# Kernel optimization log

Measured on AMD Instinct MI355X. Metric: run time of the kernel, lower is better.

## Reference

```python
import jax, jax.numpy as jnp
import numpy as np

N_EXPERTS = 8
TOP_K = 2


def setup_inputs() -> dict:
    key = jax.random.key(0)
    ks = jax.random.split(key, 5)
    B, T, C, E, H = 8, 2048, 256, 8, 682  # H = int(8/3*256)
    scale = 1.0 / np.sqrt(C)
    return {
        "x": jax.random.normal(ks[0], (B, T, C), dtype=jnp.float32),
        "router_w": jax.random.normal(ks[1], (E, C), dtype=jnp.float32) * scale,
        "w1": jax.random.normal(ks[2], (E, H, C), dtype=jnp.float32) * scale,
        "w2": jax.random.normal(ks[3], (E, C, H), dtype=jnp.float32) * (1.0 / np.sqrt(H)),
        "w3": jax.random.normal(ks[4], (E, H, C), dtype=jnp.float32) * scale,
    }


def reference(x, router_w, w1, w2, w3):
    B, T, C = x.shape
    flat = x.reshape(-1, C)  # [N, C]

    # Router: softmax over experts, top-k selection, renormalize.
    logits = flat @ router_w.T                     # [N, E]
    probs = jax.nn.softmax(logits, axis=-1)
    topk_probs, topk_idx = jax.lax.top_k(probs, TOP_K)
    topk_probs = topk_probs / (jnp.sum(topk_probs, axis=-1, keepdims=True) + 1e-9)

    # Dense gate matrix [N, E]: zero for non-selected experts (same math as
    # the masked loop, since unselected experts contribute weight 0).
    onehot = jax.nn.one_hot(topk_idx, N_EXPERTS, dtype=flat.dtype)  # [N, K, E]
    gates = jnp.einsum("nk,nke->ne", topk_probs, onehot)           # [N, E]

    # SwiGLU experts, computed densely over E and combined with gates.
    h1 = jnp.einsum("nc,ehc->neh", flat, w1)       # [N, E, H]
    h3 = jnp.einsum("nc,ehc->neh", flat, w3)       # [N, E, H]
    h = jax.nn.silu(h1) * h3                       # [N, E, H]
    y = jnp.einsum("neh,ech->nec", h, w2)          # [N, E, C]
    out = jnp.einsum("ne,nec->nc", gates, y)       # [N, C]
    return out.reshape(B, T, C)
```

## Files before the change

kernel.cpp:

```cpp
#include <hip/hip_runtime.h>
#include <hip/hip_bf16.h>

#define N_TOK 16384
#define C_DIM 256
#define E_NUM 8
#define H_DIM 682
#define H_PAD 768
#define NROWS (N_TOK * 2)
#define HB 64
#define APB (NROWS / HB)

typedef short short8 __attribute__((ext_vector_type(8)));
typedef float floatx4 __attribute__((ext_vector_type(4)));
typedef unsigned int uint;

__device__ inline unsigned short f2bf(float v) {
    union { float f; uint u; } x; x.f = v;
    uint r = (x.u + 0x7fffu + ((x.u >> 16) & 1u)) >> 16;
    return (unsigned short)r;
}
__device__ inline float bf2f(unsigned short v) {
    union { uint u; float f; } x; x.u = ((uint)v) << 16; return x.f;
}

__device__ __forceinline__ void load_lds16(const void* g, void* l) {
    __builtin_amdgcn_global_load_lds(
        (const __attribute__((address_space(1))) unsigned int*)g,
        (__attribute__((address_space(3))) unsigned int*)l, 16, 0, 0);
}

#define VMCNT6 asm volatile("s_waitcnt vmcnt(6)" ::: "memory")
#define VMCNT4 asm volatile("s_waitcnt vmcnt(4)" ::: "memory")
#define VMCNT0 asm volatile("s_waitcnt vmcnt(0)" ::: "memory")

#define P13 (E_NUM * H_PAD * (C_DIM / 2))
#define P2  (E_NUM * C_DIM * (H_PAD / 2))
__global__ void wconvert(const float* __restrict__ w1, const float* __restrict__ w3,
                         const float* __restrict__ w2, unsigned short* __restrict__ w1b,
                         unsigned short* __restrict__ w3b, unsigned short* __restrict__ w2b) {
    int idx = blockIdx.x * 256 + threadIdx.x;
    if (idx < 2 * P13) {
        const float* src = (idx < P13) ? w1 : w3;
        unsigned short* dst = (idx < P13) ? w1b : w3b;
        int i = (idx < P13) ? idx : idx - P13;
        int e = i / (H_PAD * (C_DIM / 2));
        int rem = i - e * (H_PAD * (C_DIM / 2));
        int r = rem / (C_DIM / 2);
        int c2 = rem - r * (C_DIM / 2);
        uint v = 0;
        if (r < H_DIM) {
            const float2 f = *(const float2*)(src + ((size_t)e * H_DIM + r) * C_DIM + c2 * 2);
            v = (uint)f2bf(f.x) | ((uint)f2bf(f.y) << 16);
        }
        ((uint*)dst)[i] = v;
    } else if (idx < 2 * P13 + P2) {
        int i = idx - 2 * P13;
        int e = i / (C_DIM * (H_PAD / 2));
        int rem = i - e * (C_DIM * (H_PAD / 2));
        int r = rem / (H_PAD / 2);
        int c2 = rem - r * (H_PAD / 2);
        uint v = 0;
        if (c2 * 2 < H_DIM) {
            const float2 f = *(const float2*)(w2 + ((size_t)e * C_DIM + r) * H_DIM + c2 * 2);
            v = (uint)f2bf(f.x) | ((uint)f2bf(f.y) << 16);
        }
        ((uint*)w2b)[i] = v;
    }
}

__global__ __launch_bounds__(256) void router_kernel(
    const float* __restrict__ x, const float* __restrict__ rw,
    unsigned short* __restrict__ xb, int* __restrict__ as_e, float* __restrict__ as_gate) {
    __shared__ float rws[E_NUM * C_DIM];
    int tid = threadIdx.x;
    for (int i = tid; i < E_NUM * C_DIM; i += 256) rws[i] = rw[i];
    __syncthreads();
    int wave = tid >> 6, lane = tid & 63;
    int t = blockIdx.x * 4 + wave;
    const float4 xv = *(const float4*)(x + (size_t)t * C_DIM + lane * 4);
    uint2 pk;
    pk.x = (uint)f2bf(xv.x) | ((uint)f2bf(xv.y) << 16);
    pk.y = (uint)f2bf(xv.z) | ((uint)f2bf(xv.w) << 16);
    *(uint2*)(xb + (size_t)t * C_DIM + lane * 4) = pk;
    float p[E_NUM];
#pragma unroll
    for (int e = 0; e < E_NUM; e++) {
        const float* wr = &rws[e * C_DIM + lane * 4];
        p[e] = xv.x * wr[0] + xv.y * wr[1] + xv.z * wr[2] + xv.w * wr[3];
    }
#pragma unroll
    for (int off = 32; off >= 1; off >>= 1) {
#pragma unroll
        for (int e = 0; e < E_NUM; e++) p[e] += __shfl_down(p[e], off, 64);
    }
    if (lane == 0) {
        float m = p[0];
#pragma unroll
        for (int e = 1; e < E_NUM; e++) m = fmaxf(m, p[e]);
        float s = 0.f, q[E_NUM];
#pragma unroll
        for (int e = 0; e < E_NUM; e++) { q[e] = expf(p[e] - m); s += q[e]; }
#pragma unroll
        for (int e = 0; e < E_NUM; e++) q[e] /= s;
        int e0 = 0;
#pragma unroll
        for (int e = 1; e < E_NUM; e++) if (q[e] > q[e0]) e0 = e;
        int e1 = (e0 == 0) ? 1 : 0;
#pragma unroll
        for (int e = 0; e < E_NUM; e++) {
            if (e != e0 && q[e] > q[e1]) e1 = e;
        }
        float g0 = q[e0], g1 = q[e1];
        float denom = g0 + g1 + 1e-9f;
        g0 /= denom; g1 /= denom;
        as_e[t * 2] = e0; as_gate[t * 2] = g0;
        as_e[t * 2 + 1] = e1; as_gate[t * 2 + 1] = g1;
    }
}

__global__ __launch_bounds__(256) void hist_kernel(const int* __restrict__ as_e,
                                                   int* __restrict__ block_hist) {
    __shared__ int lh[E_NUM];
    int b = blockIdx.x, tid = threadIdx.x;
    if (tid < E_NUM) lh[tid] = 0;
    __syncthreads();
    for (int i = tid; i < APB; i += 256) atomicAdd(&lh[as_e[b * APB + i]], 1);
    __syncthreads();
    if (tid < E_NUM) block_hist[b * E_NUM + tid] = lh[tid];
}

__global__ void scan2_kernel(const int* __restrict__ block_hist, int* __restrict__ offsets,
                             int* __restrict__ block_base) {
    __shared__ int tot[E_NUM], off[E_NUM];
    int e = threadIdx.x;
    if (e < E_NUM) {
        int s = 0;
        for (int b = 0; b < HB; b++) s += block_hist[b * E_NUM + e];
        tot[e] = s;
    }
    __syncthreads();
    if (e == 0) {
        int acc = 0;
        for (int i = 0; i < E_NUM; i++) { off[i] = acc; offsets[i] = acc; acc += tot[i]; }
        offsets[E_NUM] = acc;
    }
    __syncthreads();
    if (e < E_NUM) {
        int acc = off[e];
        for (int b = 0; b < HB; b++) { block_base[b * E_NUM + e] = acc; acc += block_hist[b * E_NUM + e]; }
    }
}

__global__ __launch_bounds__(256) void scatter_kernel(
    const int* __restrict__ as_e, const int* __restrict__ block_base,
    int* __restrict__ row_token, int* __restrict__ as_row) {
    __shared__ int cur[E_NUM];
    int b = blockIdx.x, tid = threadIdx.x;
    if (tid < E_NUM) cur[tid] = block_base[b * E_NUM + tid];
    __syncthreads();
    for (int i = tid; i < APB; i += 256) {
        int a = b * APB + i;
        int e = as_e[a];
        int p = atomicAdd(&cur[e], 1);
        row_token[p] = a >> 1;
        as_row[a] = p;
    }
}

__global__ __launch_bounds__(256, 2) void expert_ffn1(
    const unsigned short* __restrict__ xb, const unsigned short* __restrict__ w1b,
    const unsigned short* __restrict__ w3b, const int* __restrict__ offsets,
    const int* __restrict__ row_token, unsigned short* __restrict__ h) {
    int e = blockIdx.x >> 6;
    int mt = blockIdx.x & 63;
    int c = blockIdx.y;
    int off0 = offsets[e], off1 = offsets[e + 1];
    int row0 = off0 + mt * 128;
    if (row0 >= off1) return;
    int mval = min(128, off1 - row0);

    __shared__ union {
        unsigned short buf[3][12288];
        unsigned short Hs[128 * 136];
    } sm;

    int tid = threadIdx.x, lane = tid & 63, w = tid >> 6;
    int wm = w & 1, wn = w >> 1;
    int ra = tid >> 2;
    int acol = (((tid & 3) ^ ((ra >> 1) & 3))) * 8;
    int tok0 = row_token[row0 + min(ra, mval - 1)];
    int tok1 = row_token[row0 + min(ra + 64, mval - 1)];
    const unsigned short* a0p = xb + (size_t)tok0 * C_DIM + acol;
    const unsigned short* a1p = xb + (size_t)tok1 * C_DIM + acol;
    const unsigned short* b1p0 = w1b + ((size_t)e * H_PAD + c * 128 + ra) * C_DIM + acol;
    const unsigned short* b1p1 = b1p0 + (size_t)64 * C_DIM;
    const unsigned short* b3p0 = w3b + ((size_t)e * H_PAD + c * 128 + ra) * C_DIM + acol;
    const unsigned short* b3p1 = b3p0 + (size_t)64 * C_DIM;

    int wofs = w * 512;
    auto stage = [&](int kt, unsigned short* base) {
        int kb = kt * 32;
        load_lds16(a0p + kb, base + wofs);
        load_lds16(a1p + kb, base + 2048 + wofs);
        load_lds16(b1p0 + kb, base + 4096 + wofs);
        load_lds16(b1p1 + kb, base + 6144 + wofs);
        load_lds16(b3p0 + kb, base + 8192 + wofs);
        load_lds16(b3p1 + kb, base + 10240 + wofs);
    };

    int ko = ((lane >> 4) ^ ((lane >> 1) & 3)) * 8;
    int l15 = lane & 15;
    int arowf = wm * 64 + l15;
    int browf = wn * 64 + l15;
    int quad = lane >> 4;

    stage(0, sm.buf[0]);
    stage(1, sm.buf[1]);

    floatx4 acc1[4][4], acc3[4][4];
#pragma unroll
    for (int m = 0; m < 4; m++)
#pragma unroll
        for (int n = 0; n < 4; n++) {
            acc1[m][n] = (floatx4){0.f, 0.f, 0.f, 0.f};
            acc3[m][n] = (floatx4){0.f, 0.f, 0.f, 0.f};
        }

#pragma unroll
    for (int kt = 0; kt < 8; kt++) {
        if (kt == 7) { VMCNT0; } else { VMCNT6; }
        __builtin_amdgcn_s_barrier();
        if (kt + 2 < 8) stage(kt + 2, sm.buf[(kt + 2) % 3]);
        const unsigned short* cur = sm.buf[kt % 3];
        short8 af[4], b1f[4], b3f[4];
#pragma unroll
        for (int m = 0; m < 4; m++) af[m] = *(short8*)&cur[(arowf + m * 16) * 32 + ko];
#pragma unroll
        for (int n = 0; n < 4; n++) {
            b1f[n] = *(short8*)&cur[4096 + (browf + n * 16) * 32 + ko];
            b3f[n] = *(short8*)&cur[8192 + (browf + n * 16) * 32 + ko];
        }
        __builtin_amdgcn_s_setprio(1);
#pragma unroll
        for (int m = 0; m < 4; m++)
#pragma unroll
            for (int n = 0; n < 4; n++) {
                acc1[m][n] = __builtin_amdgcn_mfma_f32_16x16x32_bf16(af[m], b1f[n], acc1[m][n], 0, 0, 0);
                acc3[m][n] = __builtin_amdgcn_mfma_f32_16x16x32_bf16(af[m], b3f[n], acc3[m][n], 0, 0, 0);
            }
        __builtin_amdgcn_s_setprio(0);
        __builtin_amdgcn_s_barrier();
    }
    __syncthreads();

#pragma unroll
    for (int m = 0; m < 4; m++)
#pragma unroll
        for (int n = 0; n < 4; n++)
#pragma unroll
            for (int r = 0; r < 4; r++) {
                float h1 = acc1[m][n][r], h3 = acc3[m][n][r];
                float sv = h1 / (1.0f + __expf(-h1)) * h3;
                sm.Hs[(wm * 64 + m * 16 + quad * 4 + r) * 136 + wn * 64 + n * 16 + l15] = f2bf(sv);
            }
    __syncthreads();
#pragma unroll
    for (int it = 0; it < 8; it++) {
        int s = it * 256 + tid;
        int row = s >> 4, c16 = s & 15;
        if (row < mval)
            *(int4*)(h + (size_t)(row0 + row) * H_PAD + c * 128 + c16 * 8) =
                *(int4*)&sm.Hs[row * 136 + c16 * 8];
    }
}

__global__ __launch_bounds__(256, 3) void expert_ffn2(
    const unsigned short* __restrict__ h, const unsigned short* __restrict__ w2b,
    const int* __restrict__ offsets, unsigned short* __restrict__ y) {
    int e = blockIdx.x >> 6;
    int mt = blockIdx.x & 63;
    int p = blockIdx.y;
    int off0 = offsets[e], off1 = offsets[e + 1];
    int row0 = off0 + mt * 128;
    if (row0 >= off1) return;
    int mval = min(128, off1 - row0);

    __shared__ union {
        unsigned short buf[3][8192];
        unsigned short Hs[128 * 136];
    } sm;

    int tid = threadIdx.x, lane = tid & 63, w = tid >> 6;
    int wm = w & 1, wn = w >> 1;
    int ra = tid >> 2;
    int acol = (((tid & 3) ^ ((ra >> 1) & 3))) * 8;
    const unsigned short* ap0 = h + (size_t)(row0 + ra) * H_PAD + acol;
    const unsigned short* ap1 = ap0 + (size_t)64 * H_PAD;
    const unsigned short* bp0 = w2b + ((size_t)e * C_DIM + p * 128 + ra) * H_PAD + acol;
    const unsigned short* bp1 = bp0 + (size_t)64 * H_PAD;

    int wofs = w * 512;
    auto stage = [&](int kt, unsigned short* base) {
        int kb = kt * 32;
        load_lds16(ap0 + kb, base + wofs);
        load_lds16(ap1 + kb, base + 2048 + wofs);
        load_lds16(bp0 + kb, base + 4096 + wofs);
        load_lds16(bp1 + kb, base + 6144 + wofs);
    };

    int ko = ((lane >> 4) ^ ((lane >> 1) & 3)) * 8;
    int l15 = lane & 15;
    int arowf = wm * 64 + l15;
    int browf = wn * 64 + l15;
    int quad = lane >> 4;

    stage(0, sm.buf[0]);
    stage(1, sm.buf[1]);

    floatx4 acc[4][4];
#pragma unroll
    for (int m = 0; m < 4; m++)
#pragma unroll
        for (int n = 0; n < 4; n++) acc[m][n] = (floatx4){0.f, 0.f, 0.f, 0.f};

#pragma unroll
    for (int kt = 0; kt < H_PAD / 32; kt++) {
        if (kt == H_PAD / 32 - 1) { VMCNT0; } else { VMCNT4; }
        __builtin_amdgcn_s_barrier();
        if (kt + 2 < H_PAD / 32) stage(kt + 2, sm.buf[(kt + 2) % 3]);
        const unsigned short* cur = sm.buf[kt % 3];
        short8 af[4], bf[4];
#pragma unroll
        for (int m = 0; m < 4; m++) af[m] = *(short8*)&cur[(arowf + m * 16) * 32 + ko];
#pragma unroll
        for (int n = 0; n < 4; n++) bf[n] = *(short8*)&cur[4096 + (browf + n * 16) * 32 + ko];
        __builtin_amdgcn_s_setprio(1);
#pragma unroll
        for (int m = 0; m < 4; m++)
#pragma unroll
            for (int n = 0; n < 4; n++)
                acc[m][n] = __builtin_amdgcn_mfma_f32_16x16x32_bf16(af[m], bf[n], acc[m][n], 0, 0, 0);
        __builtin_amdgcn_s_setprio(0);
        __builtin_amdgcn_s_barrier();
    }
    __syncthreads();

#pragma unroll
    for (int m = 0; m < 4; m++)
#pragma unroll
        for (int n = 0; n < 4; n++)
#pragma unroll
            for (int r = 0; r < 4; r++)
                sm.Hs[(wm * 64 + m * 16 + quad * 4 + r) * 136 + wn * 64 + n * 16 + l15] =
                    f2bf(acc[m][n][r]);
    __syncthreads();
#pragma unroll
    for (int it = 0; it < 8; it++) {
        int s = it * 256 + tid;
        int row = s >> 4, c16 = s & 15;
        if (row < mval)
            *(int4*)(y + (size_t)(row0 + row) * C_DIM + p * 128 + c16 * 8) =
                *(int4*)&sm.Hs[row * 136 + c16 * 8];
    }
}

__global__ __launch_bounds__(256) void combine_kernel(
    const unsigned short* __restrict__ y, const int* __restrict__ as_row,
    const float* __restrict__ as_gate, float* __restrict__ out) {
    int tid = threadIdx.x, lane = tid & 63;
    int t = blockIdx.x * 4 + (tid >> 6);
    int r0 = as_row[2 * t], r1 = as_row[2 * t + 1];
    float g0 = as_gate[2 * t], g1 = as_gate[2 * t + 1];
    uint2 a = *(const uint2*)(y + (size_t)r0 * C_DIM + lane * 4);
    uint2 b = *(const uint2*)(y + (size_t)r1 * C_DIM + lane * 4);
    float4 o;
    o.x = g0 * bf2f((unsigned short)(a.x & 0xffff)) + g1 * bf2f((unsigned short)(b.x & 0xffff));
    o.y = g0 * bf2f((unsigned short)(a.x >> 16)) + g1 * bf2f((unsigned short)(b.x >> 16));
    o.z = g0 * bf2f((unsigned short)(a.y & 0xffff)) + g1 * bf2f((unsigned short)(b.y & 0xffff));
    o.w = g0 * bf2f((unsigned short)(a.y >> 16)) + g1 * bf2f((unsigned short)(b.y >> 16));
    *(float4*)(out + (size_t)t * C_DIM + lane * 4) = o;
}

extern "C" void kernel_launch(void* const* d_in, const int* in_sizes, int n_in,
                              void* d_out, int out_size, void* d_ws, size_t ws_size,
                              hipStream_t stream) {
    const float* x = (const float*)d_in[0];
    const float* rw = (const float*)d_in[1];
    const float* w1 = (const float*)d_in[2];
    const float* w2 = (const float*)d_in[3];
    const float* w3 = (const float*)d_in[4];
    float* out = (float*)d_out;

    char* ws = (char*)d_ws;
    size_t o = 0;
    auto alloc = [&](size_t bytes) {
        void* p = ws + o;
        o = (o + bytes + 255) & ~(size_t)255;
        return p;
    };
    unsigned short* xb = (unsigned short*)alloc((size_t)N_TOK * C_DIM * 2);
    unsigned short* w1b = (unsigned short*)alloc((size_t)E_NUM * H_PAD * C_DIM * 2);
    unsigned short* w3b = (unsigned short*)alloc((size_t)E_NUM * H_PAD * C_DIM * 2);
    unsigned short* w2b = (unsigned short*)alloc((size_t)E_NUM * C_DIM * H_PAD * 2);
    unsigned short* hbuf = (unsigned short*)alloc((size_t)(NROWS + 128) * H_PAD * 2);
    unsigned short* ybuf = (unsigned short*)alloc((size_t)NROWS * C_DIM * 2);
    int* offsets = (int*)alloc((E_NUM + 1) * 4);
    int* as_e = (int*)alloc(NROWS * 4);
    float* as_gate = (float*)alloc(NROWS * 4);
    int* row_token = (int*)alloc(NROWS * 4);
    int* as_row = (int*)alloc(NROWS * 4);
    int* block_hist = (int*)alloc(HB * E_NUM * 4);
    int* block_base = (int*)alloc(HB * E_NUM * 4);

    wconvert<<<(2 * P13 + P2 + 255) / 256, 256, 0, stream>>>(w1, w3, w2, w1b, w3b, w2b);
    router_kernel<<<N_TOK / 4, 256, 0, stream>>>(x, rw, xb, as_e, as_gate);
    hist_kernel<<<HB, 256, 0, stream>>>(as_e, block_hist);
    scan2_kernel<<<1, 64, 0, stream>>>(block_hist, offsets, block_base);
    scatter_kernel<<<HB, 256, 0, stream>>>(as_e, block_base, row_token, as_row);

    expert_ffn1<<<dim3(E_NUM * 64, 6), 256, 0, stream>>>(xb, w1b, w3b, offsets, row_token, hbuf);
    expert_ffn2<<<dim3(E_NUM * 64, 2), 256, 0, stream>>>(hbuf, w2b, offsets, ybuf);
    combine_kernel<<<N_TOK / 4, 256, 0, stream>>>(ybuf, as_row, as_gate, out);
}
```

Measured before the change: 194.8 us.

## Load GEMM A operand straight into registers, stage only weights through LDS

In both expert FFN kernels, the activation (A) tiles now go from global memory straight into double-buffered registers in MFMA fragment layout. Only the weight (B) tiles still go through LDS via global_load_lds. This shrinks the LDS staging buffers and removes the LDS write/read round trip and bank traffic for A. The vmcnt waits are retuned to the new load counts, and an lgkmcnt wait is added before the end-of-iteration barrier. In exchange, the two waves that share an A row-block each fetch it from global/L2 separately, and the register-held double buffer raises register pressure.

```diff
diff --git a/kernel.cpp b/kernel.cpp
--- a/kernel.cpp
+++ b/kernel.cpp
@@ -29,9 +29,10 @@
         (__attribute__((address_space(3))) unsigned int*)l, 16, 0, 0);
 }
 
-#define VMCNT6 asm volatile("s_waitcnt vmcnt(6)" ::: "memory")
 #define VMCNT4 asm volatile("s_waitcnt vmcnt(4)" ::: "memory")
+#define VMCNT2 asm volatile("s_waitcnt vmcnt(2)" ::: "memory")
 #define VMCNT0 asm volatile("s_waitcnt vmcnt(0)" ::: "memory")
+#define LGKM0  asm volatile("s_waitcnt lgkmcnt(0)" ::: "memory")
 
 #define P13 (E_NUM * H_PAD * (C_DIM / 2))
 #define P2  (E_NUM * C_DIM * (H_PAD / 2))
@@ -180,7 +181,7 @@
     int mval = min(128, off1 - row0);
 
     __shared__ union {
-        unsigned short buf[3][12288];
+        unsigned short buf[3][8192];
         unsigned short Hs[128 * 136];
     } sm;
 
@@ -188,34 +189,42 @@
     int wm = w & 1, wn = w >> 1;
     int ra = tid >> 2;
     int acol = (((tid & 3) ^ ((ra >> 1) & 3))) * 8;
-    int tok0 = row_token[row0 + min(ra, mval - 1)];
-    int tok1 = row_token[row0 + min(ra + 64, mval - 1)];
-    const unsigned short* a0p = xb + (size_t)tok0 * C_DIM + acol;
-    const unsigned short* a1p = xb + (size_t)tok1 * C_DIM + acol;
     const unsigned short* b1p0 = w1b + ((size_t)e * H_PAD + c * 128 + ra) * C_DIM + acol;
     const unsigned short* b1p1 = b1p0 + (size_t)64 * C_DIM;
     const unsigned short* b3p0 = w3b + ((size_t)e * H_PAD + c * 128 + ra) * C_DIM + acol;
     const unsigned short* b3p1 = b3p0 + (size_t)64 * C_DIM;
 
     int wofs = w * 512;
-    auto stage = [&](int kt, unsigned short* base) {
+    auto stageB = [&](int kt, unsigned short* base) {
         int kb = kt * 32;
-        load_lds16(a0p + kb, base + wofs);
-        load_lds16(a1p + kb, base + 2048 + wofs);
-        load_lds16(b1p0 + kb, base + 4096 + wofs);
-        load_lds16(b1p1 + kb, base + 6144 + wofs);
-        load_lds16(b3p0 + kb, base + 8192 + wofs);
-        load_lds16(b3p1 + kb, base + 10240 + wofs);
+        load_lds16(b1p0 + kb, base + wofs);
+        load_lds16(b1p1 + kb, base + 2048 + wofs);
+        load_lds16(b3p0 + kb, base + 4096 + wofs);
+        load_lds16(b3p1 + kb, base + 6144 + wofs);
     };
 
-    int ko = ((lane >> 4) ^ ((lane >> 1) & 3)) * 8;
     int l15 = lane & 15;
+    int quad = lane >> 4;
     int arowf = wm * 64 + l15;
     int browf = wn * 64 + l15;
-    int quad = lane >> 4;
-
-    stage(0, sm.buf[0]);
-    stage(1, sm.buf[1]);
+    int ko = (quad ^ ((lane >> 1) & 3)) * 8;
+
+    const unsigned short* aB[4];
+#pragma unroll
+    for (int m = 0; m < 4; m++) {
+        int arow = row0 + min(arowf + m * 16, mval - 1);
+        aB[m] = xb + (size_t)row_token[arow] * C_DIM + quad * 8;
+    }
+
+    short8 af[2][4];
+    auto ldA = [&](int kt) {
+#pragma unroll
+        for (int m = 0; m < 4; m++) af[kt & 1][m] = *(const short8*)(aB[m] + kt * 32);
+    };
+
+    ldA(0);
+    stageB(0, sm.buf[0]);
+    stageB(1, sm.buf[1]);
 
     floatx4 acc1[4][4], acc3[4][4];
 #pragma unroll
@@ -228,27 +237,27 @@
 
 #pragma unroll
     for (int kt = 0; kt < 8; kt++) {
-        if (kt == 7) { VMCNT0; } else { VMCNT6; }
+        if (kt < 7) { VMCNT4; } else { VMCNT0; }
         __builtin_amdgcn_s_barrier();
-        if (kt + 2 < 8) stage(kt + 2, sm.buf[(kt + 2) % 3]);
+        if (kt + 1 < 8) ldA(kt + 1);
+        if (kt + 2 < 8) stageB(kt + 2, sm.buf[(kt + 2) % 3]);
         const unsigned short* cur = sm.buf[kt % 3];
-        short8 af[4], b1f[4], b3f[4];
-#pragma unroll
-        for (int m = 0; m < 4; m++) af[m] = *(short8*)&cur[(arowf + m * 16) * 32 + ko];
+        short8 b1f[4], b3f[4];
 #pragma unroll
         for (int n = 0; n < 4; n++) {
-            b1f[n] = *(short8*)&cur[4096 + (browf + n * 16) * 32 + ko];
-            b3f[n] = *(short8*)&cur[8192 + (browf + n * 16) * 32 + ko];
+            b1f[n] = *(short8*)&cur[(browf + n * 16) * 32 + ko];
+            b3f[n] = *(short8*)&cur[4096 + (browf + n * 16) * 32 + ko];
         }
         __builtin_amdgcn_s_setprio(1);
 #pragma unroll
         for (int m = 0; m < 4; m++)
 #pragma unroll
             for (int n = 0; n < 4; n++) {
-                acc1[m][n] = __builtin_amdgcn_mfma_f32_16x16x32_bf16(af[m], b1f[n], acc1[m][n], 0, 0, 0);
-                acc3[m][n] = __builtin_amdgcn_mfma_f32_16x16x32_bf16(af[m], b3f[n], acc3[m][n], 0, 0, 0);
+                acc1[m][n] = __builtin_amdgcn_mfma_f32_16x16x32_bf16(af[kt & 1][m], b1f[n], acc1[m][n], 0, 0, 0);
+                acc3[m][n] = __builtin_amdgcn_mfma_f32_16x16x32_bf16(af[kt & 1][m], b3f[n], acc3[m][n], 0, 0, 0);
             }
         __builtin_amdgcn_s_setprio(0);
+        LGKM0;
         __builtin_amdgcn_s_barrier();
     }
     __syncthreads();
@@ -286,7 +295,7 @@
     int mval = min(128, off1 - row0);
 
     __shared__ union {
-        unsigned short buf[3][8192];
+        unsigned short buf[3][4096];
         unsigned short Hs[128 * 136];
     } sm;
 
@@ -294,28 +303,38 @@
     int wm = w & 1, wn = w >> 1;
     int ra = tid >> 2;
     int acol = (((tid & 3) ^ ((ra >> 1) & 3))) * 8;
-    const unsigned short* ap0 = h + (size_t)(row0 + ra) * H_PAD + acol;
-    const unsigned short* ap1 = ap0 + (size_t)64 * H_PAD;
     const unsigned short* bp0 = w2b + ((size_t)e * C_DIM + p * 128 + ra) * H_PAD + acol;
     const unsigned short* bp1 = bp0 + (size_t)64 * H_PAD;
 
     int wofs = w * 512;
-    auto stage = [&](int kt, unsigned short* base) {
+    auto stageB = [&](int kt, unsigned short* base) {
         int kb = kt * 32;
-        load_lds16(ap0 + kb, base + wofs);
-        load_lds16(ap1 + kb, base + 2048 + wofs);
-        load_lds16(bp0 + kb, base + 4096 + wofs);
-        load_lds16(bp1 + kb, base + 6144 + wofs);
+        load_lds16(bp0 + kb, base + wofs);
+        load_lds16(bp1 + kb, base + 2048 + wofs);
     };
 
-    int ko = ((lane >> 4) ^ ((lane >> 1) & 3)) * 8;
     int l15 = lane & 15;
+    int quad = lane >> 4;
     int arowf = wm * 64 + l15;
     int browf = wn * 64 + l15;
-    int quad = lane >> 4;
-
-    stage(0, sm.buf[0]);
-    stage(1, sm.buf[1]);
+    int ko = (quad ^ ((lane >> 1) & 3)) * 8;
+
+    const unsigned short* aB[4];
+#pragma unroll
+    for (int m = 0; m < 4; m++) {
+        int arow = row0 + min(arowf + m * 16, mval - 1);
+        aB[m] = h + (size_t)arow * H_PAD + quad * 8;
+    }
+
+    short8 af[2][4];
+    auto ldA = [&](int kt) {
+#pragma unroll
+        for (int m = 0; m < 4; m++) af[kt & 1][m] = *(const short8*)(aB[m] + kt * 32);
+    };
+
+    ldA(0);
+    stageB(0, sm.buf[0]);
+    stageB(1, sm.buf[1]);
 
     floatx4 acc[4][4];
 #pragma unroll
@@ -325,22 +344,22 @@
 
 #pragma unroll
     for (int kt = 0; kt < H_PAD / 32; kt++) {
-        if (kt == H_PAD / 32 - 1) { VMCNT0; } else { VMCNT4; }
+        if (kt < H_PAD / 32 - 1) { VMCNT2; } else { VMCNT0; }
         __builtin_amdgcn_s_barrier();
-        if (kt + 2 < H_PAD / 32) stage(kt + 2, sm.buf[(kt + 2) % 3]);
+        if (kt + 1 < H_PAD / 32) ldA(kt + 1);
+        if (kt + 2 < H_PAD / 32) stageB(kt + 2, sm.buf[(kt + 2) % 3]);
         const unsigned short* cur = sm.buf[kt % 3];
-        short8 af[4], bf[4];
-#pragma unroll
-        for (int m = 0; m < 4; m++) af[m] = *(short8*)&cur[(arowf + m * 16) * 32 + ko];
-#pragma unroll
-        for (int n = 0; n < 4; n++) bf[n] = *(short8*)&cur[4096 + (browf + n * 16) * 32 + ko];
+        short8 bf[4];
+#pragma unroll
+        for (int n = 0; n < 4; n++) bf[n] = *(short8*)&cur[(browf + n * 16) * 32 + ko];
         __builtin_amdgcn_s_setprio(1);
 #pragma unroll
         for (int m = 0; m < 4; m++)
 #pragma unroll
             for (int n = 0; n < 4; n++)
-                acc[m][n] = __builtin_amdgcn_mfma_f32_16x16x32_bf16(af[m], bf[n], acc[m][n], 0, 0, 0);
+                acc[m][n] = __builtin_amdgcn_mfma_f32_16x16x32_bf16(af[kt & 1][m], bf[n], acc[m][n], 0, 0, 0);
         __builtin_amdgcn_s_setprio(0);
+        LGKM0;
         __builtin_amdgcn_s_barrier();
     }
     __syncthreads();
```

Result: slower. 228.5 us (+17.3%).

## Merge weight conversion into router kernel and deepen ffn2 K-step to 64

Applied to the files above, without the earlier changes.

Folds the weight bf16 conversion and the router into one launch, with block ranges assigned to each job, removing a kernel launch and letting the two independent jobs run concurrently. In expert_ffn2 the triple-buffered 32-wide K pipeline becomes a double-buffered 64-wide K step. This halves the number of barriers per tile but doubles LDS per buffer, and occupancy is lowered to 2 blocks per SM. The prefetch is now issued before the wait, which reduces how much load latency can be hidden.

```diff
diff --git a/kernel.cpp b/kernel.cpp
--- a/kernel.cpp
+++ b/kernel.cpp
@@ -29,54 +29,58 @@
         (__attribute__((address_space(3))) unsigned int*)l, 16, 0, 0);
 }
 
+#define VMCNT8 asm volatile("s_waitcnt vmcnt(8)" ::: "memory")
 #define VMCNT6 asm volatile("s_waitcnt vmcnt(6)" ::: "memory")
-#define VMCNT4 asm volatile("s_waitcnt vmcnt(4)" ::: "memory")
 #define VMCNT0 asm volatile("s_waitcnt vmcnt(0)" ::: "memory")
+#define LGKM0  asm volatile("s_waitcnt lgkmcnt(0)" ::: "memory")
 
 #define P13 (E_NUM * H_PAD * (C_DIM / 2))
 #define P2  (E_NUM * C_DIM * (H_PAD / 2))
-__global__ void wconvert(const float* __restrict__ w1, const float* __restrict__ w3,
-                         const float* __restrict__ w2, unsigned short* __restrict__ w1b,
-                         unsigned short* __restrict__ w3b, unsigned short* __restrict__ w2b) {
-    int idx = blockIdx.x * 256 + threadIdx.x;
-    if (idx < 2 * P13) {
-        const float* src = (idx < P13) ? w1 : w3;
-        unsigned short* dst = (idx < P13) ? w1b : w3b;
-        int i = (idx < P13) ? idx : idx - P13;
-        int e = i / (H_PAD * (C_DIM / 2));
-        int rem = i - e * (H_PAD * (C_DIM / 2));
-        int r = rem / (C_DIM / 2);
-        int c2 = rem - r * (C_DIM / 2);
-        uint v = 0;
-        if (r < H_DIM) {
-            const float2 f = *(const float2*)(src + ((size_t)e * H_DIM + r) * C_DIM + c2 * 2);
-            v = (uint)f2bf(f.x) | ((uint)f2bf(f.y) << 16);
-        }
-        ((uint*)dst)[i] = v;
-    } else if (idx < 2 * P13 + P2) {
-        int i = idx - 2 * P13;
-        int e = i / (C_DIM * (H_PAD / 2));
-        int rem = i - e * (C_DIM * (H_PAD / 2));
-        int r = rem / (H_PAD / 2);
-        int c2 = rem - r * (H_PAD / 2);
-        uint v = 0;
-        if (c2 * 2 < H_DIM) {
-            const float2 f = *(const float2*)(w2 + ((size_t)e * C_DIM + r) * H_DIM + c2 * 2);
-            v = (uint)f2bf(f.x) | ((uint)f2bf(f.y) << 16);
-        }
-        ((uint*)w2b)[i] = v;
-    }
-}
-
-__global__ __launch_bounds__(256) void router_kernel(
+#define WCONV_BLKS ((2 * P13 + P2) / 256)
+
+__global__ __launch_bounds__(256) void prep_kernel(
+    const float* __restrict__ w1, const float* __restrict__ w3, const float* __restrict__ w2,
+    unsigned short* __restrict__ w1b, unsigned short* __restrict__ w3b,
+    unsigned short* __restrict__ w2b,
     const float* __restrict__ x, const float* __restrict__ rw,
     unsigned short* __restrict__ xb, int* __restrict__ as_e, float* __restrict__ as_gate) {
     __shared__ float rws[E_NUM * C_DIM];
     int tid = threadIdx.x;
+    if (blockIdx.x < WCONV_BLKS) {
+        int idx = blockIdx.x * 256 + tid;
+        if (idx < 2 * P13) {
+            const float* src = (idx < P13) ? w1 : w3;
+            unsigned short* dst = (idx < P13) ? w1b : w3b;
+            int i = (idx < P13) ? idx : idx - P13;
+            int e = i / (H_PAD * (C_DIM / 2));
+            int rem = i - e * (H_PAD * (C_DIM / 2));
+            int r = rem / (C_DIM / 2);
+            int c2 = rem - r * (C_DIM / 2);
+            uint v = 0;
+            if (r < H_DIM) {
+                const float2 f = *(const float2*)(src + ((size_t)e * H_DIM + r) * C_DIM + c2 * 2);
+                v = (uint)f2bf(f.x) | ((uint)f2bf(f.y) << 16);
+            }
+            ((uint*)dst)[i] = v;
+        } else {
+            int i = idx - 2 * P13;
+            int e = i / (C_DIM * (H_PAD / 2));
+            int rem = i - e * (C_DIM * (H_PAD / 2));
+            int r = rem / (H_PAD / 2);
+            int c2 = rem - r * (H_PAD / 2);
+            uint v = 0;
+            if (c2 * 2 < H_DIM) {
+                const float2 f = *(const float2*)(w2 + ((size_t)e * C_DIM + r) * H_DIM + c2 * 2);
+                v = (uint)f2bf(f.x) | ((uint)f2bf(f.y) << 16);
+            }
+            ((uint*)w2b)[i] = v;
+        }
+        return;
+    }
     for (int i = tid; i < E_NUM * C_DIM; i += 256) rws[i] = rw[i];
     __syncthreads();
     int wave = tid >> 6, lane = tid & 63;
-    int t = blockIdx.x * 4 + wave;
+    int t = (blockIdx.x - WCONV_BLKS) * 4 + wave;
     const float4 xv = *(const float4*)(x + (size_t)t * C_DIM + lane * 4);
     uint2 pk;
     pk.x = (uint)f2bf(xv.x) | ((uint)f2bf(xv.y) << 16);
@@ -274,7 +278,7 @@
     }
 }
 
-__global__ __launch_bounds__(256, 3) void expert_ffn2(
+__global__ __launch_bounds__(256, 2) void expert_ffn2(
     const unsigned short* __restrict__ h, const unsigned short* __restrict__ w2b,
     const int* __restrict__ offsets, unsigned short* __restrict__ y) {
     int e = blockIdx.x >> 6;
@@ -286,7 +290,7 @@
     int mval = min(128, off1 - row0);
 
     __shared__ union {
-        unsigned short buf[3][8192];
+        unsigned short buf[2][16384];
         unsigned short Hs[128 * 136];
     } sm;
 
@@ -301,11 +305,16 @@
 
     int wofs = w * 512;
     auto stage = [&](int kt, unsigned short* base) {
-        int kb = kt * 32;
-        load_lds16(ap0 + kb, base + wofs);
-        load_lds16(ap1 + kb, base + 2048 + wofs);
-        load_lds16(bp0 + kb, base + 4096 + wofs);
-        load_lds16(bp1 + kb, base + 6144 + wofs);
+        int kb = kt * 64;
+#pragma unroll
+        for (int kk = 0; kk < 2; kk++) {
+            int ks = kb + kk * 32;
+            unsigned short* b2 = base + kk * 8192;
+            load_lds16(ap0 + ks, b2 + wofs);
+            load_lds16(ap1 + ks, b2 + 2048 + wofs);
+            load_lds16(bp0 + ks, b2 + 4096 + wofs);
+            load_lds16(bp1 + ks, b2 + 6144 + wofs);
+        }
     };
 
     int ko = ((lane >> 4) ^ ((lane >> 1) & 3)) * 8;
@@ -315,7 +324,6 @@
     int quad = lane >> 4;
 
     stage(0, sm.buf[0]);
-    stage(1, sm.buf[1]);
 
     floatx4 acc[4][4];
 #pragma unroll
@@ -324,23 +332,28 @@
         for (int n = 0; n < 4; n++) acc[m][n] = (floatx4){0.f, 0.f, 0.f, 0.f};
 
 #pragma unroll
-    for (int kt = 0; kt < H_PAD / 32; kt++) {
-        if (kt == H_PAD / 32 - 1) { VMCNT0; } else { VMCNT4; }
+    for (int kt = 0; kt < H_PAD / 64; kt++) {
+        if (kt + 1 < H_PAD / 64) stage(kt + 1, sm.buf[(kt + 1) & 1]);
+        if (kt + 1 < H_PAD / 64) { VMCNT8; } else { VMCNT0; }
         __builtin_amdgcn_s_barrier();
-        if (kt + 2 < H_PAD / 32) stage(kt + 2, sm.buf[(kt + 2) % 3]);
-        const unsigned short* cur = sm.buf[kt % 3];
-        short8 af[4], bf[4];
-#pragma unroll
-        for (int m = 0; m < 4; m++) af[m] = *(short8*)&cur[(arowf + m * 16) * 32 + ko];
-#pragma unroll
-        for (int n = 0; n < 4; n++) bf[n] = *(short8*)&cur[4096 + (browf + n * 16) * 32 + ko];
-        __builtin_amdgcn_s_setprio(1);
-#pragma unroll
-        for (int m = 0; m < 4; m++)
-#pragma unroll
-            for (int n = 0; n < 4; n++)
-                acc[m][n] = __builtin_amdgcn_mfma_f32_16x16x32_bf16(af[m], bf[n], acc[m][n], 0, 0, 0);
-        __builtin_amdgcn_s_setprio(0);
+        const unsigned short* cur = sm.buf[kt & 1];
+#pragma unroll
+        for (int kk = 0; kk < 2; kk++) {
+            const unsigned short* c2 = cur + kk * 8192;
+            short8 af[4], bf[4];
+#pragma unroll
+            for (int m = 0; m < 4; m++) af[m] = *(short8*)&c2[(arowf + m * 16) * 32 + ko];
+#pragma unroll
+            for (int n = 0; n < 4; n++) bf[n] = *(short8*)&c2[4096 + (browf + n * 16) * 32 + ko];
+            __builtin_amdgcn_s_setprio(1);
+#pragma unroll
+            for (int m = 0; m < 4; m++)
+#pragma unroll
+                for (int n = 0; n < 4; n++)
+                    acc[m][n] = __builtin_amdgcn_mfma_f32_16x16x32_bf16(af[m], bf[n], acc[m][n], 0, 0, 0);
+            __builtin_amdgcn_s_setprio(0);
+        }
+        LGKM0;
         __builtin_amdgcn_s_barrier();
     }
     __syncthreads();
@@ -412,8 +425,8 @@
     int* block_hist = (int*)alloc(HB * E_NUM * 4);
     int* block_base = (int*)alloc(HB * E_NUM * 4);
 
-    wconvert<<<(2 * P13 + P2 + 255) / 256, 256, 0, stream>>>(w1, w3, w2, w1b, w3b, w2b);
-    router_kernel<<<N_TOK / 4, 256, 0, stream>>>(x, rw, xb, as_e, as_gate);
+    prep_kernel<<<WCONV_BLKS + N_TOK / 4, 256, 0, stream>>>(
+        w1, w3, w2, w1b, w3b, w2b, x, rw, xb, as_e, as_gate);
     hist_kernel<<<HB, 256, 0, stream>>>(as_e, block_hist);
     scan2_kernel<<<1, 64, 0, stream>>>(block_hist, offsets, block_base);
     scatter_kernel<<<HB, 256, 0, stream>>>(as_e, block_base, row_token, as_row);
```

Measured after the change: 194.8 us. No clear change (-0.0%).
